# Optimization experiments

Hardware: AMD Instinct MI355X
Metric: run time of the kernel (lower is better)

Reference implementation:

```python
import jax, jax.numpy as jnp
import numpy as np


def gcn_conv(x, src, dst, norm, W, b, n_nodes):
    # PyG GCNConv: out[dst] = sum_edges norm * (x @ W)[src] + b
    h = x @ W                      # [N, F_out]
    msg = h[src] * norm[:, None]   # [E', F_out] gather + scale
    out = jax.ops.segment_sum(msg, dst, num_segments=n_nodes)
    return out + b


def _gcn_norm(edge_index, n_nodes):
    # add self loops, compute symmetric normalization deg^-1/2[src]*deg^-1/2[dst]
    loop = jnp.arange(n_nodes, dtype=edge_index.dtype)
    src = jnp.concatenate([edge_index[0], loop])
    dst = jnp.concatenate([edge_index[1], loop])
    deg = jnp.zeros((n_nodes,), jnp.float32).at[dst].add(1.0)
    dinv = jnp.where(deg > 0, jax.lax.rsqrt(deg), 0.0)
    norm = dinv[src] * dinv[dst]
    return src, dst, norm


def setup_inputs() -> dict:
    key = jax.random.key(0)
    ks = jax.random.split(key, 5)
    N, E, C_in, C_out = 50000, 800000, 128, 32
    H = 2 * C_out
    x = jax.random.normal(ks[0], (N, C_in), jnp.float32)
    edge_index = jax.random.randint(ks[1], (2, E), 0, N, jnp.int64)
    s1 = 1.0 / np.sqrt(C_in)
    s2 = 1.0 / np.sqrt(H)
    W1 = jax.random.uniform(ks[2], (C_in, H), jnp.float32, -s1, s1)
    b1 = jnp.zeros((H,), jnp.float32)
    W_mu = jax.random.uniform(ks[3], (H, C_out), jnp.float32, -s2, s2)
    b_mu = jnp.zeros((C_out,), jnp.float32)
    W_ls = jax.random.uniform(ks[4], (H, C_out), jnp.float32, -s2, s2)
    b_ls = jnp.zeros((C_out,), jnp.float32)
    return {"x": x, "edge_index": edge_index, "W1": W1, "b1": b1,
            "W_mu": W_mu, "b_mu": b_mu, "W_ls": W_ls, "b_ls": b_ls}


def reference(x, edge_index, W1, b1, W_mu, b_mu, W_ls, b_ls):
    n_nodes = x.shape[0]
    src, dst, norm = _gcn_norm(edge_index, n_nodes)
    h = jax.nn.relu(gcn_conv(x, src, dst, norm, W1, b1, n_nodes))
    mu = gcn_conv(h, src, dst, norm, W_mu, b_mu, n_nodes)
    logstd = gcn_conv(h, src, dst, norm, W_ls, b_ls, n_nodes)
    return mu, logstd
```

## Files before the change

### kernel.cpp

```cpp
#include <hip/hip_runtime.h>
#include <hip/hip_fp16.h>
#include <math.h>


typedef unsigned int uint;
typedef unsigned short ushort;
typedef __attribute__((ext_vector_type(8))) short short8;
typedef __attribute__((ext_vector_type(4))) float f32x4;
typedef __attribute__((ext_vector_type(2))) float f32v2;

__device__ __forceinline__ ushort f2bf(float x) {
    uint u = __float_as_uint(x);
    u += 0x7fffu + ((u >> 16) & 1u);
    return (ushort)(u >> 16);
}
__device__ __forceinline__ float bf2f(ushort h) {
    return __uint_as_float((uint)h << 16);
}

__global__ __launch_bounds__(256) void k_hist(
        const int* __restrict__ dst, int* __restrict__ bcount, int E) {
    __shared__ int h[256];
    const int tid = threadIdx.x;
    h[tid] = 0;
    __syncthreads();
    const int base = blockIdx.x * 2048;
    #pragma unroll
    for (int k = 0; k < 8; ++k) {
        int i = base + k * 256 + tid;
        if (i < E) {
            int d = __builtin_nontemporal_load(dst + i);
            atomicAdd(&h[d >> 8], 1);
        }
    }
    __syncthreads();
    if (h[tid]) atomicAdd(&bcount[tid], h[tid]);
}

__global__ __launch_bounds__(256) void k_bscan(
        const int* __restrict__ bcount, int* __restrict__ bbase,
        int* __restrict__ bcursor, int E) {
    __shared__ int p[256];
    const int t = threadIdx.x;
    int v = bcount[t];
    p[t] = v;
    __syncthreads();
    #pragma unroll
    for (int off = 1; off < 256; off <<= 1) {
        int x = (t >= off) ? p[t - off] : 0;
        __syncthreads();
        p[t] += x;
        __syncthreads();
    }
    int excl = p[t] - v;
    bbase[t] = excl;
    bcursor[t] = excl;
    if (t == 255) bbase[256] = p[255];
}

__global__ __launch_bounds__(256) void k_scatterA(
        const int* __restrict__ src, const int* __restrict__ dst,
        int* __restrict__ bcursor, uint* __restrict__ recs, int E) {
    __shared__ int h[256];
    __shared__ int rb[256];
    const int tid = threadIdx.x;
    h[tid] = 0;
    __syncthreads();
    const int base = blockIdx.x * 2048;
    uint rec[8]; int rk[8];
    #pragma unroll
    for (int k = 0; k < 8; ++k) {
        int i = base + k * 256 + tid;
        if (i < E) {
            int s = __builtin_nontemporal_load(src + i);
            int d = __builtin_nontemporal_load(dst + i);
            int b = d >> 8;
            rec[k] = (uint)s | ((uint)(d & 255) << 16) | ((uint)b << 24);
            rk[k] = atomicAdd(&h[b], 1);
        }
    }
    __syncthreads();
    rb[tid] = h[tid] ? atomicAdd(&bcursor[tid], h[tid]) : 0;
    __syncthreads();
    #pragma unroll
    for (int k = 0; k < 8; ++k) {
        int i = base + k * 256 + tid;
        if (i < E) recs[rb[rec[k] >> 24] + rk[k]] = rec[k];
    }
}

__global__ __launch_bounds__(256) void k_phaseB(
        const uint* __restrict__ recs, const int* __restrict__ bbase,
        int* __restrict__ row_ptr, float* __restrict__ dinv,
        ushort* __restrict__ edges, int N, int E, int NBUCK) {
    __shared__ int h[256];
    __shared__ int p[256];
    const int tid = threadIdx.x;
    const int b = blockIdx.x;
    const int base = bbase[b];
    const int cnt  = bbase[b + 1] - base;
    h[tid] = 0;
    __syncthreads();
    for (int i = tid; i < cnt; i += 256)
        atomicAdd(&h[(recs[base + i] >> 16) & 255], 1);
    __syncthreads();
    int v = h[tid];
    p[tid] = v;
    __syncthreads();
    #pragma unroll
    for (int off = 1; off < 256; off <<= 1) {
        int x = (tid >= off) ? p[tid - off] : 0;
        __syncthreads();
        p[tid] += x;
        __syncthreads();
    }
    const int excl = p[tid] - v;
    const int node = b * 256 + tid;
    if (node < N) {
        row_ptr[node] = base + excl;
        dinv[node] = rsqrtf((float)(v + 1));
    }
    if (b == NBUCK - 1 && tid == 0) row_ptr[N] = E;
    h[tid] = excl;
    __syncthreads();
    for (int i = tid; i < cnt; i += 256) {
        uint r = recs[base + i];
        int dl = (r >> 16) & 255;
        int pos = atomicAdd(&h[dl], 1);
        edges[base + pos] = (ushort)(r & 0xffffu);
    }
}

__global__ __launch_bounds__(256, 4) void k_gemm(
        const float* __restrict__ x, const float* __restrict__ W1,
        const float* __restrict__ dinv, ushort* __restrict__ hp, int N) {
    const int tid = threadIdx.x;
    const int w = tid >> 6, l = tid & 63;
    const int m = l & 15, q = l >> 4;
    const int row0 = blockIdx.x * 64 + w * 16;
    const size_t arow = (size_t)min(row0 + m, N - 1);
    f32x4 acc0 = {0.f, 0.f, 0.f, 0.f}, acc1 = acc0, acc2 = acc0, acc3 = acc0;
    #pragma unroll
    for (int kc = 0; kc < 4; ++kc) {
        const int kofs = kc * 32 + q * 8;
        const float4* xr = (const float4*)(x + arow * 128 + kofs);
        float4 xa = xr[0], xb = xr[1];
        short8 a;
        a[0] = (short)f2bf(xa.x); a[1] = (short)f2bf(xa.y);
        a[2] = (short)f2bf(xa.z); a[3] = (short)f2bf(xa.w);
        a[4] = (short)f2bf(xb.x); a[5] = (short)f2bf(xb.y);
        a[6] = (short)f2bf(xb.z); a[7] = (short)f2bf(xb.w);
        short8 b0, b1, b2, b3;
        #pragma unroll
        for (int i = 0; i < 8; ++i) {
            const float* wk = W1 + (size_t)(kofs + i) * 64 + m;
            b0[i] = (short)f2bf(wk[0]);
            b1[i] = (short)f2bf(wk[16]);
            b2[i] = (short)f2bf(wk[32]);
            b3[i] = (short)f2bf(wk[48]);
        }
        acc0 = __builtin_amdgcn_mfma_f32_16x16x32_bf16(a, b0, acc0, 0, 0, 0);
        acc1 = __builtin_amdgcn_mfma_f32_16x16x32_bf16(a, b1, acc1, 0, 0, 0);
        acc2 = __builtin_amdgcn_mfma_f32_16x16x32_bf16(a, b2, acc2, 0, 0, 0);
        acc3 = __builtin_amdgcn_mfma_f32_16x16x32_bf16(a, b3, acc3, 0, 0, 0);
    }
    #pragma unroll
    for (int r = 0; r < 4; ++r) {
        int row = row0 + q * 4 + r;
        if (row >= N) continue;
        float dv = dinv[row];
        ushort* hr = hp + (size_t)row * 64 + m;
        hr[0]  = f2bf(acc0[r] * dv);
        hr[16] = f2bf(acc1[r] * dv);
        hr[32] = f2bf(acc2[r] * dv);
        hr[48] = f2bf(acc3[r] * dv);
    }
}

__device__ __forceinline__ f32v2 gather_rows(
        const uint* __restrict__ hp, const ushort* __restrict__ edges,
        int beg, int end, int E, int lane, int hl, int half) {
    f32v2 acc = {0.f, 0.f};
    for (int base = beg; base < end; base += 64) {
        int cnt = end - base; if (cnt > 64) cnt = 64;
        int mrec = (int)edges[min(base + lane, E - 1)];
        int steps = (cnt + 1) >> 1;
        for (int t = 0; t < steps; t += 8) {
            if (2 * t + 16 <= cnt) {
                #pragma unroll
                for (int i = 0; i < 8; ++i) {
                    int r = __shfl(mrec, 2 * (t + i) + half);
                    uint v = hp[(size_t)r * 32 + hl];
                    f32v2 vf;
                    vf.x = __uint_as_float(v << 16);
                    vf.y = __uint_as_float(v & 0xffff0000u);
                    acc = acc + vf;
                }
            } else {
                #pragma unroll
                for (int i = 0; i < 8; ++i) {
                    int e = 2 * (t + i) + half;
                    int r = __shfl(mrec, min(e, cnt - 1));
                    uint v = hp[(size_t)r * 32 + hl];
                    v = (e < cnt) ? v : 0u;
                    f32v2 vf;
                    vf.x = __uint_as_float(v << 16);
                    vf.y = __uint_as_float(v & 0xffff0000u);
                    acc = acc + vf;
                }
            }
        }
    }
    acc.x += __shfl_xor(acc.x, 32);
    acc.y += __shfl_xor(acc.y, 32);
    return acc;
}

__global__ __launch_bounds__(256, 8) void k_gather1(
        const uint* __restrict__ hp, const int* __restrict__ row_ptr,
        const ushort* __restrict__ edges, const float* __restrict__ dinv,
        const float* __restrict__ b1, uint* __restrict__ ho, int N, int E) {
    const int lane = threadIdx.x & 63;
    const int hl = lane & 31, half = lane >> 5;
    const int n = blockIdx.x * 4 + (threadIdx.x >> 6);
    if (n >= N) return;
    const int beg = row_ptr[n], end = row_ptr[n + 1];
    f32v2 acc = gather_rows(hp, edges, beg, end, E, lane, hl, half);
    if (half == 0) {
        const float dv = dinv[n];
        const uint sv = hp[(size_t)n * 32 + hl];
        const float2 b = ((const float2*)b1)[hl];
        float s0 = acc.x + bf2f((ushort)sv);
        float s1 = acc.y + bf2f((ushort)(sv >> 16));
        float h0 = fmaxf(fmaf(dv, s0, b.x), 0.f) * dv;
        float h1 = fmaxf(fmaf(dv, s1, b.y), 0.f) * dv;
        ho[(size_t)n * 32 + hl] = (uint)f2bf(h0) | ((uint)f2bf(h1) << 16);
    }
}

__global__ __launch_bounds__(256, 8) void k_gather2(
        const uint* __restrict__ hp, const int* __restrict__ row_ptr,
        const ushort* __restrict__ edges, const float* __restrict__ dinv,
        const float* __restrict__ Wmu, const float* __restrict__ Wls,
        const float* __restrict__ bmu, const float* __restrict__ bls,
        float* __restrict__ out, int N, int E) {
    __shared__ float hs[4][64];
    const int lane = threadIdx.x & 63;
    const int hl = lane & 31, half = lane >> 5;
    const int w = threadIdx.x >> 6;
    const int n = blockIdx.x * 4 + w;
    if (n >= N) return;
    const int beg = row_ptr[n], end = row_ptr[n + 1];
    f32v2 acc = gather_rows(hp, edges, beg, end, E, lane, hl, half);
    if (half == 0) {
        const float dv = dinv[n];
        const uint sv = hp[(size_t)n * 32 + hl];
        float g0 = dv * (acc.x + bf2f((ushort)sv));
        float g1 = dv * (acc.y + bf2f((ushort)(sv >> 16)));
        float2 p; p.x = g0; p.y = g1;
        *(float2*)&hs[w][2 * hl] = p;
    }
    const float* Wsel = (lane < 32) ? (Wmu + lane) : (Wls + (lane - 32));
    const float bias  = (lane < 32) ? bmu[lane] : bls[lane - 32];
    float c0 = 0.f, c1 = 0.f, c2 = 0.f, c3 = 0.f;
    #pragma unroll 4
    for (int k = 0; k < 64; k += 4) {
        c0 = fmaf(hs[w][k + 0], Wsel[(k + 0) * 32], c0);
        c1 = fmaf(hs[w][k + 1], Wsel[(k + 1) * 32], c1);
        c2 = fmaf(hs[w][k + 2], Wsel[(k + 2) * 32], c2);
        c3 = fmaf(hs[w][k + 3], Wsel[(k + 3) * 32], c3);
    }
    float t = (c0 + c1) + (c2 + c3) + bias;
    if (lane < 32) out[(size_t)n * 32 + lane] = t;
    else           out[(size_t)N * 32 + (size_t)n * 32 + (lane - 32)] = t;
}

extern "C" void kernel_launch(void* const* d_in, const int* in_sizes, int n_in,
                              void* d_out, int out_size, void* d_ws, size_t ws_size,
                              hipStream_t stream) {
    const float* x   = (const float*)d_in[0];
    const int*   ei  = (const int*)d_in[1];
    const float* W1  = (const float*)d_in[2];
    const float* b1  = (const float*)d_in[3];
    const float* Wmu = (const float*)d_in[4];
    const float* bmu = (const float*)d_in[5];
    const float* Wls = (const float*)d_in[6];
    const float* bls = (const float*)d_in[7];
    float* out = (float*)d_out;

    const int N = in_sizes[0] / 128;
    const int E = in_sizes[1] / 2;
    const int* src = ei;
    const int* dst = ei + E;
    const int HB    = (E + 2047) / 2048;
    const int NBUCK = (N + 255) / 256;
    const int GB    = (N + 63) / 64;
    const int NG    = (N + 3) / 4;

    char* w = (char*)d_ws;
    auto carve = [&](size_t bytes) { char* p = w; w += (bytes + 1023) & ~(size_t)1023; return p; };
    int*    bcount  = (int*)   carve(256 * 4);
    int*    bbase   = (int*)   carve(257 * 4);
    int*    bcursor = (int*)   carve(256 * 4);
    uint*   recs    = (uint*)  carve((size_t)E * 4);
    int*    row_ptr = (int*)   carve((size_t)(N + 1) * 4);
    float*  dinv    = (float*) carve((size_t)N * 4);
    ushort* edges   = (ushort*)carve((size_t)E * 2);
    ushort* h_pre   = (ushort*)carve((size_t)N * 64 * 2);
    ushort* h_mid   = (ushort*)carve((size_t)N * 64 * 2);

    hipMemsetAsync(bcount, 0, 256 * 4, stream);
    k_hist    <<<HB, 256, 0, stream>>>(dst, bcount, E);
    k_bscan   <<<1, 256, 0, stream>>>(bcount, bbase, bcursor, E);
    k_scatterA<<<HB, 256, 0, stream>>>(src, dst, bcursor, recs, E);
    k_phaseB  <<<NBUCK, 256, 0, stream>>>(recs, bbase, row_ptr, dinv, edges, N, E, NBUCK);
    k_gemm    <<<GB, 256, 0, stream>>>(x, W1, dinv, h_pre, N);
    k_gather1 <<<NG, 256, 0, stream>>>((const uint*)h_pre, row_ptr, edges, dinv,
                                       b1, (uint*)h_mid, N, E);
    k_gather2 <<<NG, 256, 0, stream>>>((const uint*)h_mid, row_ptr, edges, dinv,
                                       Wmu, Wls, bmu, bls, out, N, E);
}
```

Measured before the change: 195.8 us.

## Fuse CSR build into one cooperative kernel and widen the gather to four edges per wave

The four CSR-construction kernels (histogram, bucket scan, bucket scatter, per-bucket sort) become one cooperative kernel that uses grid-wide syncs, and each bucket's records are staged in LDS so the second pass does not reread them from global memory. This removes several launches and their global round trips, but it relies on every block being resident at once, which needs 2 blocks per CU and a large LDS allocation. The gather kernels now process four edges per wave step, with 16 lanes each loading 8 bytes of a row, which raises memory-level parallelism at the cost of extra shuffle reductions. Occupancy hints for the gather kernels drop from 8 to 6 blocks.

Result: slower. 339.8 us (+73.6%).

```diff
diff --git a/kernel.cpp b/kernel.cpp
--- a/kernel.cpp
+++ b/kernel.cpp
@@ -1,13 +1,15 @@
 #include <hip/hip_runtime.h>
 #include <hip/hip_fp16.h>
+#include <hip/hip_cooperative_groups.h>
 #include <math.h>
+
+namespace cg = cooperative_groups;
 
 
 typedef unsigned int uint;
 typedef unsigned short ushort;
 typedef __attribute__((ext_vector_type(8))) short short8;
 typedef __attribute__((ext_vector_type(4))) float f32x4;
-typedef __attribute__((ext_vector_type(2))) float f32v2;
 
 __device__ __forceinline__ ushort f2bf(float x) {
     uint u = __float_as_uint(x);
@@ -18,59 +20,28 @@
     return __uint_as_float((uint)h << 16);
 }
 
-__global__ __launch_bounds__(256) void k_hist(
-        const int* __restrict__ dst, int* __restrict__ bcount, int E) {
+__global__ __launch_bounds__(256, 2) void k_build(
+        const int* __restrict__ src, const int* __restrict__ dst,
+        int* __restrict__ bcount, int* __restrict__ bcursor,
+        uint* __restrict__ recs, int* __restrict__ row_ptr,
+        float* __restrict__ dinv, ushort* __restrict__ edges,
+        int N, int E, int NBUCK) {
     __shared__ int h[256];
+    __shared__ int p[256];
+    __shared__ uint rstage[8192];
+    __shared__ int s_base, s_cnt;
     const int tid = threadIdx.x;
+    const int bx  = blockIdx.x;
+    cg::grid_group grid = cg::this_grid();
+
     h[tid] = 0;
     __syncthreads();
-    const int base = blockIdx.x * 2048;
+    uint rec[8]; int rk[8];
+    const int base = bx * 2048;
     #pragma unroll
     for (int k = 0; k < 8; ++k) {
         int i = base + k * 256 + tid;
-        if (i < E) {
-            int d = __builtin_nontemporal_load(dst + i);
-            atomicAdd(&h[d >> 8], 1);
-        }
-    }
-    __syncthreads();
-    if (h[tid]) atomicAdd(&bcount[tid], h[tid]);
-}
-
-__global__ __launch_bounds__(256) void k_bscan(
-        const int* __restrict__ bcount, int* __restrict__ bbase,
-        int* __restrict__ bcursor, int E) {
-    __shared__ int p[256];
-    const int t = threadIdx.x;
-    int v = bcount[t];
-    p[t] = v;
-    __syncthreads();
-    #pragma unroll
-    for (int off = 1; off < 256; off <<= 1) {
-        int x = (t >= off) ? p[t - off] : 0;
-        __syncthreads();
-        p[t] += x;
-        __syncthreads();
-    }
-    int excl = p[t] - v;
-    bbase[t] = excl;
-    bcursor[t] = excl;
-    if (t == 255) bbase[256] = p[255];
-}
-
-__global__ __launch_bounds__(256) void k_scatterA(
-        const int* __restrict__ src, const int* __restrict__ dst,
-        int* __restrict__ bcursor, uint* __restrict__ recs, int E) {
-    __shared__ int h[256];
-    __shared__ int rb[256];
-    const int tid = threadIdx.x;
-    h[tid] = 0;
-    __syncthreads();
-    const int base = blockIdx.x * 2048;
-    uint rec[8]; int rk[8];
-    #pragma unroll
-    for (int k = 0; k < 8; ++k) {
-        int i = base + k * 256 + tid;
+        rk[k] = 0;
         if (i < E) {
             int s = __builtin_nontemporal_load(src + i);
             int d = __builtin_nontemporal_load(dst + i);
@@ -80,31 +51,11 @@
         }
     }
     __syncthreads();
-    rb[tid] = h[tid] ? atomicAdd(&bcursor[tid], h[tid]) : 0;
-    __syncthreads();
-    #pragma unroll
-    for (int k = 0; k < 8; ++k) {
-        int i = base + k * 256 + tid;
-        if (i < E) recs[rb[rec[k] >> 24] + rk[k]] = rec[k];
-    }
-}
-
-__global__ __launch_bounds__(256) void k_phaseB(
-        const uint* __restrict__ recs, const int* __restrict__ bbase,
-        int* __restrict__ row_ptr, float* __restrict__ dinv,
-        ushort* __restrict__ edges, int N, int E, int NBUCK) {
-    __shared__ int h[256];
-    __shared__ int p[256];
-    const int tid = threadIdx.x;
-    const int b = blockIdx.x;
-    const int base = bbase[b];
-    const int cnt  = bbase[b + 1] - base;
-    h[tid] = 0;
-    __syncthreads();
-    for (int i = tid; i < cnt; i += 256)
-        atomicAdd(&h[(recs[base + i] >> 16) & 255], 1);
-    __syncthreads();
-    int v = h[tid];
+    const int hv = h[tid];
+    if (hv) atomicAdd(&bcount[tid], hv);
+    grid.sync();
+
+    int v = bcount[tid];
     p[tid] = v;
     __syncthreads();
     #pragma unroll
@@ -114,20 +65,57 @@
         p[tid] += x;
         __syncthreads();
     }
+    const int myExcl = p[tid] - v;
+    const int myCnt  = v;
+    int rb_ = myExcl + (hv ? atomicAdd(&bcursor[tid], hv) : 0);
+    __syncthreads();
+    p[tid] = rb_;
+    __syncthreads();
+    #pragma unroll
+    for (int k = 0; k < 8; ++k) {
+        int i = base + k * 256 + tid;
+        if (i < E) recs[p[rec[k] >> 24] + rk[k]] = rec[k];
+    }
+    __threadfence();
+    grid.sync();
+    if (bx >= NBUCK) return;
+
+    if (tid == bx) { s_base = myExcl; s_cnt = myCnt; }
+    __syncthreads();
+    const int bs  = s_base;
+    const int cnt = s_cnt;
+    h[tid] = 0;
+    __syncthreads();
+    const bool stg = (cnt <= 8192);
+    for (int i = tid; i < cnt; i += 256) {
+        uint r = recs[bs + i];
+        if (stg) rstage[i] = r;
+        atomicAdd(&h[(r >> 16) & 255], 1);
+    }
+    __syncthreads();
+    v = h[tid];
+    p[tid] = v;
+    __syncthreads();
+    #pragma unroll
+    for (int off = 1; off < 256; off <<= 1) {
+        int x = (tid >= off) ? p[tid - off] : 0;
+        __syncthreads();
+        p[tid] += x;
+        __syncthreads();
+    }
     const int excl = p[tid] - v;
-    const int node = b * 256 + tid;
+    const int node = bx * 256 + tid;
     if (node < N) {
-        row_ptr[node] = base + excl;
+        row_ptr[node] = bs + excl;
         dinv[node] = rsqrtf((float)(v + 1));
     }
-    if (b == NBUCK - 1 && tid == 0) row_ptr[N] = E;
+    if (bx == NBUCK - 1 && tid == 0) row_ptr[N] = E;
     h[tid] = excl;
     __syncthreads();
     for (int i = tid; i < cnt; i += 256) {
-        uint r = recs[base + i];
-        int dl = (r >> 16) & 255;
-        int pos = atomicAdd(&h[dl], 1);
-        edges[base + pos] = (ushort)(r & 0xffffu);
+        uint r = stg ? rstage[i] : recs[bs + i];
+        int pos = atomicAdd(&h[(r >> 16) & 255], 1);
+        edges[bs + pos] = (ushort)(r & 0xffffu);
     }
 }
 
@@ -177,88 +165,103 @@
     }
 }
 
-__device__ __forceinline__ f32v2 gather_rows(
+__device__ __forceinline__ f32x4 gather_rows4(
         const uint* __restrict__ hp, const ushort* __restrict__ edges,
-        int beg, int end, int E, int lane, int hl, int half) {
-    f32v2 acc = {0.f, 0.f};
+        int beg, int end, int E, int lane, int ql, int q) {
+    f32x4 acc = {0.f, 0.f, 0.f, 0.f};
     for (int base = beg; base < end; base += 64) {
         int cnt = end - base; if (cnt > 64) cnt = 64;
         int mrec = (int)edges[min(base + lane, E - 1)];
-        int steps = (cnt + 1) >> 1;
+        int steps = (cnt + 3) >> 2;
         for (int t = 0; t < steps; t += 8) {
-            if (2 * t + 16 <= cnt) {
+            if (4 * t + 32 <= cnt) {
                 #pragma unroll
                 for (int i = 0; i < 8; ++i) {
-                    int r = __shfl(mrec, 2 * (t + i) + half);
-                    uint v = hp[(size_t)r * 32 + hl];
-                    f32v2 vf;
-                    vf.x = __uint_as_float(v << 16);
-                    vf.y = __uint_as_float(v & 0xffff0000u);
+                    int r = __shfl(mrec, 4 * (t + i) + q);
+                    uint2 v = *(const uint2*)(hp + (size_t)r * 32 + 2 * ql);
+                    f32x4 vf;
+                    vf.x = __uint_as_float(v.x << 16);
+                    vf.y = __uint_as_float(v.x & 0xffff0000u);
+                    vf.z = __uint_as_float(v.y << 16);
+                    vf.w = __uint_as_float(v.y & 0xffff0000u);
                     acc = acc + vf;
                 }
             } else {
                 #pragma unroll
                 for (int i = 0; i < 8; ++i) {
-                    int e = 2 * (t + i) + half;
+                    int e = 4 * (t + i) + q;
                     int r = __shfl(mrec, min(e, cnt - 1));
-                    uint v = hp[(size_t)r * 32 + hl];
-                    v = (e < cnt) ? v : 0u;
-                    f32v2 vf;
-                    vf.x = __uint_as_float(v << 16);
-                    vf.y = __uint_as_float(v & 0xffff0000u);
+                    uint2 v = *(const uint2*)(hp + (size_t)r * 32 + 2 * ql);
+                    if (e >= cnt) { v.x = 0u; v.y = 0u; }
+                    f32x4 vf;
+                    vf.x = __uint_as_float(v.x << 16);
+                    vf.y = __uint_as_float(v.x & 0xffff0000u);
+                    vf.z = __uint_as_float(v.y << 16);
+                    vf.w = __uint_as_float(v.y & 0xffff0000u);
                     acc = acc + vf;
                 }
             }
         }
     }
-    acc.x += __shfl_xor(acc.x, 32);
-    acc.y += __shfl_xor(acc.y, 32);
+    acc.x += __shfl_xor(acc.x, 16); acc.y += __shfl_xor(acc.y, 16);
+    acc.z += __shfl_xor(acc.z, 16); acc.w += __shfl_xor(acc.w, 16);
+    acc.x += __shfl_xor(acc.x, 32); acc.y += __shfl_xor(acc.y, 32);
+    acc.z += __shfl_xor(acc.z, 32); acc.w += __shfl_xor(acc.w, 32);
     return acc;
 }
 
-__global__ __launch_bounds__(256, 8) void k_gather1(
+__global__ __launch_bounds__(256, 6) void k_gather1(
         const uint* __restrict__ hp, const int* __restrict__ row_ptr,
         const ushort* __restrict__ edges, const float* __restrict__ dinv,
         const float* __restrict__ b1, uint* __restrict__ ho, int N, int E) {
     const int lane = threadIdx.x & 63;
-    const int hl = lane & 31, half = lane >> 5;
+    const int ql = lane & 15, q = lane >> 4;
     const int n = blockIdx.x * 4 + (threadIdx.x >> 6);
     if (n >= N) return;
     const int beg = row_ptr[n], end = row_ptr[n + 1];
-    f32v2 acc = gather_rows(hp, edges, beg, end, E, lane, hl, half);
-    if (half == 0) {
+    f32x4 acc = gather_rows4(hp, edges, beg, end, E, lane, ql, q);
+    if (q == 0) {
         const float dv = dinv[n];
-        const uint sv = hp[(size_t)n * 32 + hl];
-        const float2 b = ((const float2*)b1)[hl];
-        float s0 = acc.x + bf2f((ushort)sv);
-        float s1 = acc.y + bf2f((ushort)(sv >> 16));
+        uint2 sv = *(const uint2*)(hp + (size_t)n * 32 + 2 * ql);
+        float4 b = ((const float4*)b1)[ql];
+        float s0 = acc.x + bf2f((ushort)sv.x);
+        float s1 = acc.y + bf2f((ushort)(sv.x >> 16));
+        float s2 = acc.z + bf2f((ushort)sv.y);
+        float s3 = acc.w + bf2f((ushort)(sv.y >> 16));
         float h0 = fmaxf(fmaf(dv, s0, b.x), 0.f) * dv;
         float h1 = fmaxf(fmaf(dv, s1, b.y), 0.f) * dv;
-        ho[(size_t)n * 32 + hl] = (uint)f2bf(h0) | ((uint)f2bf(h1) << 16);
-    }
-}
-
-__global__ __launch_bounds__(256, 8) void k_gather2(
+        float h2 = fmaxf(fmaf(dv, s2, b.z), 0.f) * dv;
+        float h3 = fmaxf(fmaf(dv, s3, b.w), 0.f) * dv;
+        uint2 o;
+        o.x = (uint)f2bf(h0) | ((uint)f2bf(h1) << 16);
+        o.y = (uint)f2bf(h2) | ((uint)f2bf(h3) << 16);
+        *(uint2*)(ho + (size_t)n * 32 + 2 * ql) = o;
+    }
+}
+
+__global__ __launch_bounds__(256, 6) void k_gather2(
         const uint* __restrict__ hp, const int* __restrict__ row_ptr,
         const ushort* __restrict__ edges, const float* __restrict__ dinv,
         const float* __restrict__ Wmu, const float* __restrict__ Wls,
         const float* __restrict__ bmu, const float* __restrict__ bls,
         float* __restrict__ out, int N, int E) {
-    __shared__ float hs[4][64];
+    __shared__ __align__(16) float hs[4][64];
     const int lane = threadIdx.x & 63;
-    const int hl = lane & 31, half = lane >> 5;
+    const int ql = lane & 15, q = lane >> 4;
     const int w = threadIdx.x >> 6;
     const int n = blockIdx.x * 4 + w;
     if (n >= N) return;
     const int beg = row_ptr[n], end = row_ptr[n + 1];
-    f32v2 acc = gather_rows(hp, edges, beg, end, E, lane, hl, half);
-    if (half == 0) {
+    f32x4 acc = gather_rows4(hp, edges, beg, end, E, lane, ql, q);
+    if (q == 0) {
         const float dv = dinv[n];
-        const uint sv = hp[(size_t)n * 32 + hl];
-        float g0 = dv * (acc.x + bf2f((ushort)sv));
-        float g1 = dv * (acc.y + bf2f((ushort)(sv >> 16)));
-        float2 p; p.x = g0; p.y = g1;
-        *(float2*)&hs[w][2 * hl] = p;
+        uint2 sv = *(const uint2*)(hp + (size_t)n * 32 + 2 * ql);
+        float4 g;
+        g.x = dv * (acc.x + bf2f((ushort)sv.x));
+        g.y = dv * (acc.y + bf2f((ushort)(sv.x >> 16)));
+        g.z = dv * (acc.z + bf2f((ushort)sv.y));
+        g.w = dv * (acc.w + bf2f((ushort)(sv.y >> 16)));
+        *(float4*)&hs[w][4 * ql] = g;
     }
     const float* Wsel = (lane < 32) ? (Wmu + lane) : (Wls + (lane - 32));
     const float bias  = (lane < 32) ? bmu[lane] : bls[lane - 32];
@@ -299,9 +302,8 @@
 
     char* w = (char*)d_ws;
     auto carve = [&](size_t bytes) { char* p = w; w += (bytes + 1023) & ~(size_t)1023; return p; };
-    int*    bcount  = (int*)   carve(256 * 4);
-    int*    bbase   = (int*)   carve(257 * 4);
-    int*    bcursor = (int*)   carve(256 * 4);
+    int*    bcount  = (int*)   carve(512 * 4);
+    int*    bcursor = bcount + 256;
     uint*   recs    = (uint*)  carve((size_t)E * 4);
     int*    row_ptr = (int*)   carve((size_t)(N + 1) * 4);
     float*  dinv    = (float*) carve((size_t)N * 4);
@@ -309,11 +311,14 @@
     ushort* h_pre   = (ushort*)carve((size_t)N * 64 * 2);
     ushort* h_mid   = (ushort*)carve((size_t)N * 64 * 2);
 
-    hipMemsetAsync(bcount, 0, 256 * 4, stream);
-    k_hist    <<<HB, 256, 0, stream>>>(dst, bcount, E);
-    k_bscan   <<<1, 256, 0, stream>>>(bcount, bbase, bcursor, E);
-    k_scatterA<<<HB, 256, 0, stream>>>(src, dst, bcursor, recs, E);
-    k_phaseB  <<<NBUCK, 256, 0, stream>>>(recs, bbase, row_ptr, dinv, edges, N, E, NBUCK);
+    hipMemsetAsync(bcount, 0, 512 * 4, stream);
+
+    int N_ = N, E_ = E, NBUCK_ = NBUCK;
+    void* kargs[] = {(void*)&src, (void*)&dst, (void*)&bcount, (void*)&bcursor,
+                     (void*)&recs, (void*)&row_ptr, (void*)&dinv, (void*)&edges,
+                     (void*)&N_, (void*)&E_, (void*)&NBUCK_};
+    hipLaunchCooperativeKernel(k_build, dim3(HB), dim3(256), kargs, 0, stream);
+
     k_gemm    <<<GB, 256, 0, stream>>>(x, W1, dinv, h_pre, N);
     k_gather1 <<<NG, 256, 0, stream>>>((const uint*)h_pre, row_ptr, edges, dinv,
                                        b1, (uint*)h_mid, N, E);
```
